# Kernel tuning notes

Hardware: AMD Instinct MI355X
Metric: run time of the kernel (lower is better)

## Reference

```python
import jax, jax.numpy as jnp
import numpy as np

N, C, H, E = 51200, 200, 128, 8
NE = N * 32
S_COEF, B_COEF = 0.01, 0.01
BN_EPS = 1e-5


def setup_inputs() -> dict:
    key = jax.random.key(0)
    ks = jax.random.split(key, 12)
    inp = {}
    inp["v"] = jax.random.normal(ks[0], (N, C), jnp.float32)
    inp["a_rows"] = jax.random.randint(ks[1], (NE,), 0, N, dtype=jnp.int32)
    inp["a_cols"] = jax.random.randint(ks[2], (NE,), 0, N, dtype=jnp.int32)
    inp["a_vals"] = jax.random.uniform(ks[3], (NE,), jnp.float32)
    inp["gate_W"] = jax.random.normal(ks[4], (C, E), jnp.float32) * 0.05
    inp["gate_b"] = jnp.zeros((E,), jnp.float32)
    inp["eps"] = jnp.zeros((E,), jnp.float32)  # GIN epsilon, init 0
    inp["W1"] = jax.random.normal(ks[5], (E, C, H), jnp.float32) / np.sqrt(C)
    inp["b1"] = jnp.zeros((E, H), jnp.float32)
    inp["g1"] = jnp.ones((E, H), jnp.float32)
    inp["beta1"] = jnp.zeros((E, H), jnp.float32)
    inp["W2"] = jax.random.normal(ks[6], (E, H, H), jnp.float32) / np.sqrt(H)
    inp["b2"] = jnp.zeros((E, H), jnp.float32)
    inp["g2"] = jnp.ones((E, H), jnp.float32)
    inp["beta2"] = jnp.zeros((E, H), jnp.float32)
    inp["b"] = 4
    inp["t"] = 64
    inp["n"] = 200
    return inp


def _bn_relu(h, g, beta):
    # h: [E, N, H]; batch-norm over node axis per expert (training-mode batch stats)
    mu = jnp.mean(h, axis=1, keepdims=True)
    var = jnp.var(h, axis=1, keepdims=True)
    hn = (h - mu) * jax.lax.rsqrt(var + BN_EPS)
    return jax.nn.relu(hn * g[:, None, :] + beta[:, None, :])


def reference(v, a_rows, a_cols, a_vals, gate_W, gate_b, eps,
              W1, b1, g1, beta1, W2, b2, g2, beta2, b, t, n):
    num_nodes, c = v.shape
    e = gate_W.shape[1]
    # ---- gating on x = rearrange(v, '(b t n) c -> b t n c') ----
    x = v.reshape(b, t, n, c)
    logits = jnp.einsum('btnc,ce->btne', x, gate_W) + gate_b
    probs = jax.nn.softmax(logits, axis=-1)                 # [b,t,n,E]
    top_val = jnp.max(probs, axis=-1, keepdims=True)
    top_idx = jnp.argmax(probs, axis=-1)
    gates = jax.nn.one_hot(top_idx, e, dtype=probs.dtype) * top_val  # top-1 sparse gates
    # ---- aux losses (switch-style balance; sparsity = mean top prob) ----
    probs_flat = probs.reshape(-1, e)
    gates_flat = gates.reshape(-1, e)
    importance = jnp.mean(probs_flat, axis=0)
    load = jnp.mean(jax.nn.one_hot(top_idx.reshape(-1), e, dtype=probs.dtype), axis=0)
    bal_loss = B_COEF * e * jnp.sum(importance * load)
    spa_loss = -S_COEF * jnp.mean(top_val)
    # ---- all-expert GIN compute (dense over experts, as in the torch loop) ----
    # shared sparse aggregation: agg[i] = sum_j a[i,j] * v[j]
    agg = jax.ops.segment_sum(a_vals[:, None] * v[a_cols], a_rows, num_segments=num_nodes)
    xin = agg[None] + (1.0 + eps)[:, None, None] * v[None]  # [E,N,C]
    h = jnp.einsum('enc,ech->enh', xin, W1) + b1[:, None, :]
    h = _bn_relu(h, g1, beta1)
    h = jnp.einsum('enk,ekh->enh', h, W2) + b2[:, None, :]
    h = _bn_relu(h, g2, beta2)                               # [E,N,H]
    # ---- gate-masked combine ----
    out = jnp.einsum('enh,ne->nh', h, gates_flat)            # [N,H]
    return out, (bal_loss, spa_loss)
```

## Files before the change

kernel.cpp:

```cpp
#include <hip/hip_runtime.h>


#define NNODES 51200
#define CDIM   200
#define CPAD   208
#define HDIM   128
#define NEXP   8
#define BNEPS  1e-5f
#define KC1    26
#define KS2    8
#define NB     400
#define CAP    6144
#define EPB    8192

typedef __attribute__((ext_vector_type(8)))  short short8;
typedef __attribute__((ext_vector_type(16))) float floatx16;
typedef unsigned short ushort_t;

__device__ __forceinline__ ushort_t f2bf(float x) {
  unsigned int u = __float_as_uint(x);
  u += 0x7fffu + ((u >> 16) & 1u);
  return (ushort_t)(u >> 16);
}
__device__ __forceinline__ float bf2f(ushort_t h) {
  return __uint_as_float(((unsigned int)h) << 16);
}

__global__ __launch_bounds__(256) void gating_kernel(
    const float* __restrict__ v, const float* __restrict__ gW,
    const float* __restrict__ gb, int* __restrict__ top_idx,
    float* __restrict__ top_val, ushort_t* __restrict__ v_bf,
    float* __restrict__ imp_acc, float* __restrict__ cnt_acc,
    float* __restrict__ tv_acc)
{
  __shared__ float s_imp[NEXP], s_cnt[NEXP], s_tv;
  const int tid = threadIdx.x, lane = tid & 63, wave = tid >> 6;
  if (tid < NEXP) { s_imp[tid] = 0.f; s_cnt[tid] = 0.f; }
  if (tid == 0) s_tv = 0.f;
  __syncthreads();
  const int c0 = lane * 4;
  const bool act = lane < 50;
  float gwr[4][NEXP];
#pragma unroll
  for (int r = 0; r < 4; ++r)
#pragma unroll
    for (int e = 0; e < NEXP; ++e)
      gwr[r][e] = act ? gW[(c0 + r) * NEXP + e] : 0.f;
  for (int i = 0; i < 16; ++i) {
    const int node = blockIdx.x * 64 + wave * 16 + i;
    float4 x = make_float4(0.f, 0.f, 0.f, 0.f);
    if (act) x = *(const float4*)(v + (size_t)node * CDIM + c0);
    float p[NEXP];
#pragma unroll
    for (int e = 0; e < NEXP; ++e)
      p[e] = fmaf(x.x, gwr[0][e],
             fmaf(x.y, gwr[1][e],
             fmaf(x.z, gwr[2][e], x.w * gwr[3][e])));
#pragma unroll
    for (int off = 32; off > 0; off >>= 1)
#pragma unroll
      for (int e = 0; e < NEXP; ++e) p[e] += __shfl_xor(p[e], off, 64);
#pragma unroll
    for (int e = 0; e < NEXP; ++e) p[e] += gb[e];
    if (lane < 52) {
      ushort4 o = {0, 0, 0, 0};
      if (act) { o.x = f2bf(x.x); o.y = f2bf(x.y); o.z = f2bf(x.z); o.w = f2bf(x.w); }
      *(ushort4*)(v_bf + (size_t)node * CPAD + c0) = o;
    }
    float mx = p[0]; int ai = 0;
#pragma unroll
    for (int e = 1; e < NEXP; ++e) if (p[e] > mx) { mx = p[e]; ai = e; }
    float se = 0.f, pe[NEXP];
#pragma unroll
    for (int e = 0; e < NEXP; ++e) { pe[e] = __expf(p[e] - mx); se += pe[e]; }
    const float inv = 1.f / se;
    if (lane == 0) {
      top_idx[node] = ai;
      top_val[node] = inv;
#pragma unroll
      for (int e = 0; e < NEXP; ++e) atomicAdd(&s_imp[e], pe[e] * inv);
      atomicAdd(&s_cnt[ai], 1.f);
      atomicAdd(&s_tv, inv);
    }
  }
  __syncthreads();
  if (tid < NEXP) { atomicAdd(&imp_acc[tid], s_imp[tid]); atomicAdd(&cnt_acc[tid], s_cnt[tid]); }
  if (tid == 0) atomicAdd(tv_acc, s_tv);
}

__global__ __launch_bounds__(256) void bucketA_kernel(
    const int* __restrict__ rows, const int* __restrict__ cols,
    const float* __restrict__ vals, int* __restrict__ bcnt,
    int2* __restrict__ tmp, int ne)
{
  __shared__ int cnt[NB];
  __shared__ int gbase[NB];
  const int tid = threadIdx.x;
  const int base = blockIdx.x * EPB;
  for (int b = tid; b < NB; b += 256) cnt[b] = 0;
  __syncthreads();
#pragma unroll 4
  for (int j = 0; j < EPB / 256; ++j) {
    const int i = base + j * 256 + tid;
    if (i < ne) atomicAdd(&cnt[rows[i] >> 7], 1);
  }
  __syncthreads();
  for (int b = tid; b < NB; b += 256) {
    const int c = cnt[b];
    gbase[b] = c ? (b * CAP + atomicAdd(&bcnt[b], c)) : 0;
    cnt[b] = 0;
  }
  __syncthreads();
#pragma unroll 4
  for (int j = 0; j < EPB / 256; ++j) {
    const int i = base + j * 256 + tid;
    if (i < ne) {
      const int r = rows[i];
      const int b = r >> 7;
      const int pos = gbase[b] + atomicAdd(&cnt[b], 1);
      tmp[pos] = make_int2((r << 16) | cols[i], __float_as_int(vals[i]));
    }
  }
}

__global__ __launch_bounds__(256) void bucketB_kernel(
    const int2* __restrict__ tmp, const int* __restrict__ bcnt,
    int2* __restrict__ cv, int* __restrict__ row_start, int* __restrict__ counts)
{
  __shared__ int lhist[128];
  __shared__ int lcur[128];
  const int tid = threadIdx.x;
  const int b = blockIdx.x;
  const int n = bcnt[b];
  const int base = b * CAP;
  int2 ed[CAP / 256];
#pragma unroll
  for (int j = 0; j < CAP / 256; ++j) {
    const int i = j * 256 + tid;
    if (i < n) ed[j] = tmp[base + i];
  }
  if (tid < 128) lhist[tid] = 0;
  __syncthreads();
#pragma unroll
  for (int j = 0; j < CAP / 256; ++j)
    if (j * 256 + tid < n)
      atomicAdd(&lhist[(((unsigned)ed[j].x) >> 16) & 127], 1);
  __syncthreads();
  if (tid == 0) {
    int acc = base;
    for (int r = 0; r < 128; ++r) { lcur[r] = acc; acc += lhist[r]; }
  }
  __syncthreads();
  if (tid < 128) {
    row_start[(b << 7) + tid] = lcur[tid];
    counts[(b << 7) + tid] = lhist[tid];
  }
  __syncthreads();
#pragma unroll
  for (int j = 0; j < CAP / 256; ++j)
    if (j * 256 + tid < n) {
      const int r = (((unsigned)ed[j].x) >> 16) & 127;
      const int pos = atomicAdd(&lcur[r], 1);
      cv[pos] = make_int2(ed[j].x & 0xffff, ed[j].y);
    }
}

__global__ __launch_bounds__(256) void aggregate_kernel(
    const ushort_t* __restrict__ v_bf, const int2* __restrict__ cv,
    const int* __restrict__ row_start, const int* __restrict__ counts,
    ushort_t* __restrict__ agg_bf)
{
  const int node = (blockIdx.x * 256 + threadIdx.x) >> 6;
  const int lane = threadIdx.x & 63;
  const int start = row_start[node];
  const int cnt   = counts[node];
  const bool act  = lane < 52;
  float4 a = make_float4(0.f, 0.f, 0.f, 0.f);
  int k = 0;
  for (; k + 8 <= cnt; k += 8) {
    int2 ee[8];
#pragma unroll
    for (int u = 0; u < 8; ++u) ee[u] = cv[start + k + u];
    ushort4 xx[8];
#pragma unroll
    for (int u = 0; u < 8; ++u) {
      ushort4 t = {0, 0, 0, 0};
      if (act) t = *(const ushort4*)(v_bf + (size_t)ee[u].x * CPAD + lane * 4);
      xx[u] = t;
    }
#pragma unroll
    for (int u = 0; u < 8; ++u) {
      const float vv = __int_as_float(ee[u].y);
      a.x = fmaf(vv, bf2f(xx[u].x), a.x);
      a.y = fmaf(vv, bf2f(xx[u].y), a.y);
      a.z = fmaf(vv, bf2f(xx[u].z), a.z);
      a.w = fmaf(vv, bf2f(xx[u].w), a.w);
    }
  }
  for (; k < cnt; ++k) {
    const int2 e0 = cv[start + k];
    ushort4 x0 = {0, 0, 0, 0};
    if (act) x0 = *(const ushort4*)(v_bf + (size_t)e0.x * CPAD + lane * 4);
    const float v0 = __int_as_float(e0.y);
    a.x = fmaf(v0, bf2f(x0.x), a.x); a.y = fmaf(v0, bf2f(x0.y), a.y);
    a.z = fmaf(v0, bf2f(x0.z), a.z); a.w = fmaf(v0, bf2f(x0.w), a.w);
  }
  if (act) {
    ushort4 o; o.x = f2bf(a.x); o.y = f2bf(a.y); o.z = f2bf(a.z); o.w = f2bf(a.w);
    *(ushort4*)(agg_bf + (size_t)node * CPAD + lane * 4) = o;
  }
}

__global__ __launch_bounds__(256) void btconv_all(
    const float* __restrict__ W1, const float* __restrict__ W2,
    const float* __restrict__ eps, ushort_t* __restrict__ Bt1,
    ushort_t* __restrict__ Bt2)
{
  const int e = blockIdx.y, j = blockIdx.x;
  __shared__ float tile[16][128];
  const int tid = threadIdx.x;
  const int kr = tid >> 5, n4 = (tid & 31) * 4;
  const float* W; int K, jj; float sc; ushort_t* dst;
  if (j < KC1) {
    sc = (j >= 13) ? (1.f + eps[e]) : 1.f;
    jj = (j >= 13) ? (j - 13) : j;
    W = W1; K = CDIM;
    dst = Bt1 + (((size_t)e * KC1 + j) * 256) * 8;
  } else {
    sc = 1.f; jj = j - KC1; W = W2; K = HDIM;
    dst = Bt2 + (((size_t)e * KS2 + jj) * 256) * 8;
  }
#pragma unroll
  for (int h = 0; h < 2; ++h) {
    const int k = jj * 16 + kr + h * 8;
    float4 val = make_float4(0.f, 0.f, 0.f, 0.f);
    if (k < K) val = *(const float4*)(W + ((size_t)e * K + k) * HDIM + n4);
    *(float4*)&tile[kr + h * 8][n4] = val;
  }
  __syncthreads();
  const int kh = tid >> 7, n = tid & 127;
  short8 pk;
#pragma unroll
  for (int q = 0; q < 8; ++q) pk[q] = (short)f2bf(sc * tile[kh * 8 + q][n]);
  *(short8*)(dst + (size_t)tid * 8) = pk;
}

__global__ __launch_bounds__(256, 2) void gemm1_mfma(
    const ushort_t* __restrict__ agg_bf, const ushort_t* __restrict__ v_bf,
    const ushort_t* __restrict__ Bt1x, ushort_t* __restrict__ h1,
    float* __restrict__ sum1, float* __restrict__ sq1)
{
  const int m0 = blockIdx.x * 64;
  __shared__ ushort_t sA[52 * 64 * 8];
  const int tid = threadIdx.x;
  const int lane = tid & 63, wid = tid >> 6;
  const int l31 = lane & 31, half = lane >> 5;

#pragma unroll
  for (int it = 0; it < 13; ++it) {
    const int l = it * 256 + tid;
    const int g = l >> 6, m = l & 63;
    const ushort_t* src = (g < 26)
        ? agg_bf + (size_t)(m0 + m) * CPAD + g * 8
        : v_bf  + (size_t)(m0 + m) * CPAD + (g - 26) * 8;
    *(short8*)(sA + (size_t)l * 8) = *(const short8*)src;
  }
  __syncthreads();

#pragma unroll
  for (int ei = 0; ei < 2; ++ei) {
    const int e = wid + ei * 4;
    floatx16 acc[2][4];
#pragma unroll
    for (int ms = 0; ms < 2; ++ms)
#pragma unroll
      for (int ns = 0; ns < 4; ++ns)
#pragma unroll
        for (int r = 0; r < 16; ++r) acc[ms][ns][r] = 0.f;

    const ushort_t* bte = Bt1x + ((size_t)e * KC1 * 256 + half * 128 + l31) * 8;
    short8 nb[4];
#pragma unroll
    for (int ns = 0; ns < 4; ++ns)
      nb[ns] = *(const short8*)(bte + (size_t)(ns * 32) * 8);
#pragma unroll
    for (int j = 0; j < KC1; ++j) {
      short8 b[4];
#pragma unroll
      for (int ns = 0; ns < 4; ++ns) b[ns] = nb[ns];
      if (j < KC1 - 1) {
#pragma unroll
        for (int ns = 0; ns < 4; ++ns)
          nb[ns] = *(const short8*)(bte + (size_t)((j + 1) * 256 + ns * 32) * 8);
      }
      short8 a[2];
#pragma unroll
      for (int ms = 0; ms < 2; ++ms)
        a[ms] = *(const short8*)(sA + (size_t)((2 * j + half) * 64 + ms * 32 + l31) * 8);
#pragma unroll
      for (int ms = 0; ms < 2; ++ms)
#pragma unroll
        for (int ns = 0; ns < 4; ++ns)
          acc[ms][ns] = __builtin_amdgcn_mfma_f32_32x32x16_bf16(
              a[ms], b[ns], acc[ms][ns], 0, 0, 0);
    }

    ushort_t* h1e = h1 + ((size_t)e * NNODES + m0) * HDIM;
#pragma unroll
    for (int ns = 0; ns < 4; ++ns) {
      const int col = ns * 32 + l31;
      float s = 0.f, q = 0.f;
#pragma unroll
      for (int ms = 0; ms < 2; ++ms) {
#pragma unroll
        for (int r = 0; r < 16; ++r) {
          const int row = ms * 32 + (r & 3) + 8 * (r >> 2) + 4 * half;
          const float x = acc[ms][ns][r];
          h1e[(size_t)row * HDIM + col] = f2bf(x);
          s += x; q = fmaf(x, x, q);
        }
      }
      s += __shfl_xor(s, 32, 64);
      q += __shfl_xor(q, 32, 64);
      if (half == 0) {
        atomicAdd(&sum1[e * HDIM + col], s);
        atomicAdd(&sq1[e * HDIM + col], q);
      }
    }
  }
}

__global__ __launch_bounds__(256, 4) void gemm2_mfma(
    const ushort_t* __restrict__ h1, const ushort_t* __restrict__ Bt2,
    const float* __restrict__ sum1, const float* __restrict__ sq1,
    const float* __restrict__ g1, const float* __restrict__ beta1,
    const int* __restrict__ top_idx, float* __restrict__ h2_sel,
    float* __restrict__ sum2, float* __restrict__ sq2)
{
  const int e = blockIdx.y;
  const int m0 = blockIdx.x * 128;
  __shared__ ushort_t sA[16 * 129 * 8];
  __shared__ float ssum[HDIM], ssq[HDIM];
  __shared__ float sSc[HDIM], sSh[HDIM];
  __shared__ int sTop[128];
  const int tid = threadIdx.x;
  const int lane = tid & 63, wid = tid >> 6;
  const int wm = wid >> 1, wn = wid & 1;
  const int l31 = lane & 31, half = lane >> 5;
  if (tid < HDIM) {
    ssum[tid] = 0.f; ssq[tid] = 0.f;
    sTop[tid] = top_idx[m0 + tid];
    const int i = e * HDIM + tid;
    const float invN = 1.f / (float)NNODES;
    const float mean = sum1[i] * invN;
    const float var  = sq1[i] * invN - mean * mean;
    const float sc = rsqrtf(var + BNEPS) * g1[i];
    sSc[tid] = sc;
    sSh[tid] = fmaf(-mean, sc, beta1[i]);
  }
  __syncthreads();
  {
    const int g = tid & 15, r0 = tid >> 4;
    const float4 sc0 = *(const float4*)&sSc[g * 8];
    const float4 sc1 = *(const float4*)&sSc[g * 8 + 4];
    const float4 sh0 = *(const float4*)&sSh[g * 8];
    const float4 sh1 = *(const float4*)&sSh[g * 8 + 4];
#pragma unroll
    for (int c = 0; c < 8; ++c) {
      const int m = c * 16 + r0;
      const short8 hq = *(const short8*)(
          h1 + ((size_t)e * NNODES + m0 + m) * HDIM + g * 8);
      short8 pk;
      pk[0] = (short)f2bf(fmaxf(0.f, fmaf(bf2f((ushort_t)hq[0]), sc0.x, sh0.x)));
      pk[1] = (short)f2bf(fmaxf(0.f, fmaf(bf2f((ushort_t)hq[1]), sc0.y, sh0.y)));
      pk[2] = (short)f2bf(fmaxf(0.f, fmaf(bf2f((ushort_t)hq[2]), sc0.z, sh0.z)));
      pk[3] = (short)f2bf(fmaxf(0.f, fmaf(bf2f((ushort_t)hq[3]), sc0.w, sh0.w)));
      pk[4] = (short)f2bf(fmaxf(0.f, fmaf(bf2f((ushort_t)hq[4]), sc1.x, sh1.x)));
      pk[5] = (short)f2bf(fmaxf(0.f, fmaf(bf2f((ushort_t)hq[5]), sc1.y, sh1.y)));
      pk[6] = (short)f2bf(fmaxf(0.f, fmaf(bf2f((ushort_t)hq[6]), sc1.z, sh1.z)));
      pk[7] = (short)f2bf(fmaxf(0.f, fmaf(bf2f((ushort_t)hq[7]), sc1.w, sh1.w)));
      *(short8*)(sA + (size_t)(g * 129 + m) * 8) = pk;
    }
  }
  __syncthreads();

  floatx16 acc[2][2];
#pragma unroll
  for (int i = 0; i < 2; ++i)
#pragma unroll
    for (int j = 0; j < 2; ++j)
#pragma unroll
      for (int r = 0; r < 16; ++r) acc[i][j][r] = 0.f;

  const ushort_t* bte = Bt2 + ((size_t)e * KS2 * 256 + half * 128 + wn * 64 + l31) * 8;
  short8 nb0 = *(const short8*)(bte);
  short8 nb1 = *(const short8*)(bte + 32 * 8);
#pragma unroll
  for (int ks = 0; ks < KS2; ++ks) {
    const short8 b0 = nb0, b1 = nb1;
    if (ks < KS2 - 1) {
      nb0 = *(const short8*)(bte + (size_t)((ks + 1) * 256) * 8);
      nb1 = *(const short8*)(bte + (size_t)((ks + 1) * 256 + 32) * 8);
    }
    const short8 a0 = *(const short8*)(sA + (size_t)((2 * ks + half) * 129 + wm * 64 + l31) * 8);
    const short8 a1 = *(const short8*)(sA + (size_t)((2 * ks + half) * 129 + wm * 64 + 32 + l31) * 8);
    acc[0][0] = __builtin_amdgcn_mfma_f32_32x32x16_bf16(a0, b0, acc[0][0], 0, 0, 0);
    acc[0][1] = __builtin_amdgcn_mfma_f32_32x32x16_bf16(a0, b1, acc[0][1], 0, 0, 0);
    acc[1][0] = __builtin_amdgcn_mfma_f32_32x32x16_bf16(a1, b0, acc[1][0], 0, 0, 0);
    acc[1][1] = __builtin_amdgcn_mfma_f32_32x32x16_bf16(a1, b1, acc[1][1], 0, 0, 0);
  }

#pragma unroll
  for (int ms = 0; ms < 2; ++ms)
#pragma unroll
    for (int ns = 0; ns < 2; ++ns) {
      const int col = wn * 64 + ns * 32 + l31;
      float s = 0.f, q = 0.f;
#pragma unroll
      for (int r = 0; r < 16; ++r) {
        const int row = wm * 64 + ms * 32 + (r & 3) + 8 * (r >> 2) + 4 * half;
        const float x = acc[ms][ns][r];
        if (sTop[row] == e) h2_sel[(size_t)(m0 + row) * HDIM + col] = x;
        s += x; q = fmaf(x, x, q);
      }
      atomicAdd(&ssum[col], s);
      atomicAdd(&ssq[col], q);
    }
  __syncthreads();
  if (tid < HDIM) atomicAdd(&sum2[e * HDIM + tid], ssum[tid]);
  else            atomicAdd(&sq2[e * HDIM + tid - HDIM], ssq[tid - HDIM]);
}

__global__ __launch_bounds__(256) void combine_kernel(
    const float* __restrict__ h2_sel, const int* __restrict__ top_idx,
    const float* __restrict__ top_val, const float* __restrict__ sum2,
    const float* __restrict__ sq2, const float* __restrict__ g2,
    const float* __restrict__ beta2, const float* __restrict__ imp,
    const float* __restrict__ cntv, const float* __restrict__ tv,
    float* __restrict__ out)
{
  __shared__ float s2[NEXP * HDIM], b2s[NEXP * HDIM];
  const int tid = threadIdx.x;
  const float invN = 1.f / (float)NNODES;
  for (int t = tid; t < NEXP * HDIM; t += 256) {
    const float mean = sum2[t] * invN;
    const float var  = sq2[t] * invN - mean * mean;
    const float sc = rsqrtf(var + BNEPS) * g2[t];
    s2[t] = sc;
    b2s[t] = fmaf(-mean, sc, beta2[t]);
  }
  __syncthreads();
  const int i4 = (blockIdx.x * 256 + tid) * 4;
  const int n = i4 >> 7, h = i4 & 127;
  const int e = top_idx[n];
  const float tvv = top_val[n];
  const float4 x = *(const float4*)(h2_sel + i4);
  const float* sc = s2 + e * HDIM + h;
  const float* sh = b2s + e * HDIM + h;
  float4 o;
  o.x = tvv * fmaxf(0.f, fmaf(x.x, sc[0], sh[0]));
  o.y = tvv * fmaxf(0.f, fmaf(x.y, sc[1], sh[1]));
  o.z = tvv * fmaxf(0.f, fmaf(x.z, sc[2], sh[2]));
  o.w = tvv * fmaxf(0.f, fmaf(x.w, sc[3], sh[3]));
  *(float4*)(out + i4) = o;
  if (blockIdx.x == 0 && tid == 0) {
    float bal = 0.f;
#pragma unroll
    for (int q = 0; q < NEXP; ++q) bal += (imp[q] * invN) * (cntv[q] * invN);
    out[(size_t)NNODES * HDIM]     = 0.01f * (float)NEXP * bal;
    out[(size_t)NNODES * HDIM + 1] = -0.01f * tv[0] * invN;
  }
}

struct WS {
  ushort_t *v_bf, *agg_bf, *h1, *Bt1x, *Bt2;
  float *h2_sel;
  int2 *cv, *tmp;
  int *row_start, *counts, *top_idx;
  float *top_val;
  char *zero_base; size_t zero_bytes;
  int *bcnt;
  float *sum1, *sq1, *sum2, *sq2, *imp, *cnt, *tv;
  size_t total;
};

static WS carve_ws(char* base)
{
  WS w; size_t off = 0;
  auto take = [&](size_t b) -> char* {
    char* r = base + off; off += (b + 255) & ~(size_t)255; return r;
  };
  w.v_bf   = (ushort_t*)take((size_t)NNODES * CPAD * 2);
  w.agg_bf = (ushort_t*)take((size_t)NNODES * CPAD * 2);
  w.h2_sel = (float*)w.v_bf;
  w.h1     = (ushort_t*)take((size_t)NEXP * NNODES * HDIM * 2);
  w.cv     = (int2*)take((size_t)NB * CAP * 8);
  w.tmp    = (int2*)take((size_t)NB * CAP * 8);
  w.Bt1x   = (ushort_t*)take((size_t)NEXP * KC1 * 2048 * 2);
  w.Bt2    = (ushort_t*)take((size_t)NEXP * KS2 * 2048 * 2);
  w.row_start = (int*)take(NNODES * 4);
  w.counts    = (int*)take(NNODES * 4);
  w.top_idx   = (int*)take(NNODES * 4);
  w.top_val   = (float*)take(NNODES * 4);
  w.zero_base = base + off;
  w.bcnt = (int*)take(NB * 4);
  w.sum1 = (float*)take(NEXP * HDIM * 4);
  w.sq1  = (float*)take(NEXP * HDIM * 4);
  w.sum2 = (float*)take(NEXP * HDIM * 4);
  w.sq2  = (float*)take(NEXP * HDIM * 4);
  w.imp  = (float*)take(NEXP * 4);
  w.cnt  = (float*)take(NEXP * 4);
  w.tv   = (float*)take(4);
  w.zero_bytes = (size_t)((base + off) - w.zero_base);
  w.total = off;
  return w;
}

extern "C" void kernel_launch(void* const* d_in, const int* in_sizes, int n_in,
                              void* d_out, int out_size, void* d_ws, size_t ws_size,
                              hipStream_t stream)
{
  const float* v      = (const float*)d_in[0];
  const int*   a_rows = (const int*)d_in[1];
  const int*   a_cols = (const int*)d_in[2];
  const float* a_vals = (const float*)d_in[3];
  const float* gate_W = (const float*)d_in[4];
  const float* gate_b = (const float*)d_in[5];
  const float* eps    = (const float*)d_in[6];
  const float* W1     = (const float*)d_in[7];
  const float* g1     = (const float*)d_in[9];
  const float* beta1  = (const float*)d_in[10];
  const float* W2     = (const float*)d_in[11];
  const float* g2     = (const float*)d_in[13];
  const float* beta2  = (const float*)d_in[14];
  const int NE = in_sizes[1];
  float* out = (float*)d_out;
  (void)n_in; (void)out_size; (void)ws_size;

  WS w = carve_ws((char*)d_ws);

  hipMemsetAsync(w.zero_base, 0, w.zero_bytes, stream);

  gating_kernel<<<NNODES / 64, 256, 0, stream>>>(
      v, gate_W, gate_b, w.top_idx, w.top_val, w.v_bf, w.imp, w.cnt, w.tv);
  btconv_all<<<dim3(KC1 + KS2, NEXP), 256, 0, stream>>>(
      W1, W2, eps, w.Bt1x, w.Bt2);
  bucketA_kernel<<<(NE + EPB - 1) / EPB, 256, 0, stream>>>(
      a_rows, a_cols, a_vals, w.bcnt, w.tmp, NE);
  bucketB_kernel<<<NB, 256, 0, stream>>>(
      w.tmp, w.bcnt, w.cv, w.row_start, w.counts);
  aggregate_kernel<<<NNODES / 4, 256, 0, stream>>>(
      w.v_bf, w.cv, w.row_start, w.counts, w.agg_bf);

  gemm1_mfma<<<NNODES / 64, 256, 0, stream>>>(
      w.agg_bf, w.v_bf, w.Bt1x, w.h1, w.sum1, w.sq1);
  gemm2_mfma<<<dim3(NNODES / 128, NEXP), 256, 0, stream>>>(
      w.h1, w.Bt2, w.sum1, w.sq1, g1, beta1, w.top_idx,
      w.h2_sel, w.sum2, w.sq2);
  combine_kernel<<<(NNODES * HDIM) / 1024, 256, 0, stream>>>(
      w.h2_sel, w.top_idx, w.top_val, w.sum2, w.sq2, g2, beta2,
      w.imp, w.cnt, w.tv, out);
}
```

Measured before the change: 543.7 us.

## Fuse sparse neighbor aggregation into gemm1 shared-memory prologue

Removes the standalone aggregate kernel and computes each node's sparse neighbor sum directly into gemm1's shared-memory A tile, alongside the node's own features, using a row-major padded layout. This avoids writing and re-reading the bf16 aggregate buffer in global memory and one kernel launch. In exchange, the latency-bound gathers now run inside the GEMM blocks with fewer waves in flight and a smaller unroll, which may hurt latency hiding. h2_sel gets its own buffer instead of aliasing v_bf.

```diff
diff --git a/kernel.cpp b/kernel.cpp
--- a/kernel.cpp
+++ b/kernel.cpp
@@ -12,6 +12,7 @@
 #define NB     400
 #define CAP    6144
 #define EPB    8192
+#define ASTR   428
 
 typedef __attribute__((ext_vector_type(8)))  short short8;
 typedef __attribute__((ext_vector_type(16))) float floatx16;
@@ -163,52 +164,6 @@
       const int pos = atomicAdd(&lcur[r], 1);
       cv[pos] = make_int2(ed[j].x & 0xffff, ed[j].y);
     }
-}
-
-__global__ __launch_bounds__(256) void aggregate_kernel(
-    const ushort_t* __restrict__ v_bf, const int2* __restrict__ cv,
-    const int* __restrict__ row_start, const int* __restrict__ counts,
-    ushort_t* __restrict__ agg_bf)
-{
-  const int node = (blockIdx.x * 256 + threadIdx.x) >> 6;
-  const int lane = threadIdx.x & 63;
-  const int start = row_start[node];
-  const int cnt   = counts[node];
-  const bool act  = lane < 52;
-  float4 a = make_float4(0.f, 0.f, 0.f, 0.f);
-  int k = 0;
-  for (; k + 8 <= cnt; k += 8) {
-    int2 ee[8];
-#pragma unroll
-    for (int u = 0; u < 8; ++u) ee[u] = cv[start + k + u];
-    ushort4 xx[8];
-#pragma unroll
-    for (int u = 0; u < 8; ++u) {
-      ushort4 t = {0, 0, 0, 0};
-      if (act) t = *(const ushort4*)(v_bf + (size_t)ee[u].x * CPAD + lane * 4);
-      xx[u] = t;
-    }
-#pragma unroll
-    for (int u = 0; u < 8; ++u) {
-      const float vv = __int_as_float(ee[u].y);
-      a.x = fmaf(vv, bf2f(xx[u].x), a.x);
-      a.y = fmaf(vv, bf2f(xx[u].y), a.y);
-      a.z = fmaf(vv, bf2f(xx[u].z), a.z);
-      a.w = fmaf(vv, bf2f(xx[u].w), a.w);
-    }
-  }
-  for (; k < cnt; ++k) {
-    const int2 e0 = cv[start + k];
-    ushort4 x0 = {0, 0, 0, 0};
-    if (act) x0 = *(const ushort4*)(v_bf + (size_t)e0.x * CPAD + lane * 4);
-    const float v0 = __int_as_float(e0.y);
-    a.x = fmaf(v0, bf2f(x0.x), a.x); a.y = fmaf(v0, bf2f(x0.y), a.y);
-    a.z = fmaf(v0, bf2f(x0.z), a.z); a.w = fmaf(v0, bf2f(x0.w), a.w);
-  }
-  if (act) {
-    ushort4 o; o.x = f2bf(a.x); o.y = f2bf(a.y); o.z = f2bf(a.z); o.w = f2bf(a.w);
-    *(ushort4*)(agg_bf + (size_t)node * CPAD + lane * 4) = o;
-  }
 }
 
 __global__ __launch_bounds__(256) void btconv_all(
@@ -246,24 +201,63 @@
 }
 
 __global__ __launch_bounds__(256, 2) void gemm1_mfma(
-    const ushort_t* __restrict__ agg_bf, const ushort_t* __restrict__ v_bf,
+    const ushort_t* __restrict__ v_bf, const int2* __restrict__ cv,
+    const int* __restrict__ row_start, const int* __restrict__ counts,
     const ushort_t* __restrict__ Bt1x, ushort_t* __restrict__ h1,
     float* __restrict__ sum1, float* __restrict__ sq1)
 {
   const int m0 = blockIdx.x * 64;
-  __shared__ ushort_t sA[52 * 64 * 8];
+  __shared__ ushort_t sA[64 * ASTR];
   const int tid = threadIdx.x;
   const int lane = tid & 63, wid = tid >> 6;
   const int l31 = lane & 31, half = lane >> 5;
-
-#pragma unroll
-  for (int it = 0; it < 13; ++it) {
-    const int l = it * 256 + tid;
-    const int g = l >> 6, m = l & 63;
-    const ushort_t* src = (g < 26)
-        ? agg_bf + (size_t)(m0 + m) * CPAD + g * 8
-        : v_bf  + (size_t)(m0 + m) * CPAD + (g - 26) * 8;
-    *(short8*)(sA + (size_t)l * 8) = *(const short8*)src;
+  const bool act = lane < 52;
+
+  for (int rr = 0; rr < 16; ++rr) {
+    const int m = wid * 16 + rr;
+    const int node = m0 + m;
+    if (act)
+      *(ushort4*)(sA + (size_t)m * ASTR + 208 + lane * 4) =
+          *(const ushort4*)(v_bf + (size_t)node * CPAD + lane * 4);
+    const int start = row_start[node];
+    const int cnt   = counts[node];
+    float4 a = make_float4(0.f, 0.f, 0.f, 0.f);
+    int k = 0;
+    for (; k + 4 <= cnt; k += 4) {
+      const int2 e0 = cv[start + k];
+      const int2 e1 = cv[start + k + 1];
+      const int2 e2 = cv[start + k + 2];
+      const int2 e3 = cv[start + k + 3];
+      ushort4 x0 = {0,0,0,0}, x1 = {0,0,0,0}, x2 = {0,0,0,0}, x3 = {0,0,0,0};
+      if (act) {
+        x0 = *(const ushort4*)(v_bf + (size_t)e0.x * CPAD + lane * 4);
+        x1 = *(const ushort4*)(v_bf + (size_t)e1.x * CPAD + lane * 4);
+        x2 = *(const ushort4*)(v_bf + (size_t)e2.x * CPAD + lane * 4);
+        x3 = *(const ushort4*)(v_bf + (size_t)e3.x * CPAD + lane * 4);
+      }
+      const float v0 = __int_as_float(e0.y), v1 = __int_as_float(e1.y);
+      const float v2 = __int_as_float(e2.y), v3 = __int_as_float(e3.y);
+      a.x = fmaf(v0, bf2f(x0.x), a.x); a.y = fmaf(v0, bf2f(x0.y), a.y);
+      a.z = fmaf(v0, bf2f(x0.z), a.z); a.w = fmaf(v0, bf2f(x0.w), a.w);
+      a.x = fmaf(v1, bf2f(x1.x), a.x); a.y = fmaf(v1, bf2f(x1.y), a.y);
+      a.z = fmaf(v1, bf2f(x1.z), a.z); a.w = fmaf(v1, bf2f(x1.w), a.w);
+      a.x = fmaf(v2, bf2f(x2.x), a.x); a.y = fmaf(v2, bf2f(x2.y), a.y);
+      a.z = fmaf(v2, bf2f(x2.z), a.z); a.w = fmaf(v2, bf2f(x2.w), a.w);
+      a.x = fmaf(v3, bf2f(x3.x), a.x); a.y = fmaf(v3, bf2f(x3.y), a.y);
+      a.z = fmaf(v3, bf2f(x3.z), a.z); a.w = fmaf(v3, bf2f(x3.w), a.w);
+    }
+    for (; k < cnt; ++k) {
+      const int2 e0 = cv[start + k];
+      ushort4 x0 = {0, 0, 0, 0};
+      if (act) x0 = *(const ushort4*)(v_bf + (size_t)e0.x * CPAD + lane * 4);
+      const float v0 = __int_as_float(e0.y);
+      a.x = fmaf(v0, bf2f(x0.x), a.x); a.y = fmaf(v0, bf2f(x0.y), a.y);
+      a.z = fmaf(v0, bf2f(x0.z), a.z); a.w = fmaf(v0, bf2f(x0.w), a.w);
+    }
+    if (act) {
+      ushort4 o; o.x = f2bf(a.x); o.y = f2bf(a.y); o.z = f2bf(a.z); o.w = f2bf(a.w);
+      *(ushort4*)(sA + (size_t)m * ASTR + lane * 4) = o;
+    }
   }
   __syncthreads();
 
@@ -296,7 +290,7 @@
       short8 a[2];
 #pragma unroll
       for (int ms = 0; ms < 2; ++ms)
-        a[ms] = *(const short8*)(sA + (size_t)((2 * j + half) * 64 + ms * 32 + l31) * 8);
+        a[ms] = *(const short8*)(sA + (size_t)(ms * 32 + l31) * ASTR + (2 * j + half) * 8);
 #pragma unroll
       for (int ms = 0; ms < 2; ++ms)
 #pragma unroll
@@ -473,7 +467,7 @@
 }
 
 struct WS {
-  ushort_t *v_bf, *agg_bf, *h1, *Bt1x, *Bt2;
+  ushort_t *v_bf, *h1, *Bt1x, *Bt2;
   float *h2_sel;
   int2 *cv, *tmp;
   int *row_start, *counts, *top_idx;
@@ -491,8 +485,7 @@
     char* r = base + off; off += (b + 255) & ~(size_t)255; return r;
   };
   w.v_bf   = (ushort_t*)take((size_t)NNODES * CPAD * 2);
-  w.agg_bf = (ushort_t*)take((size_t)NNODES * CPAD * 2);
-  w.h2_sel = (float*)w.v_bf;
+  w.h2_sel = (float*)take((size_t)NNODES * HDIM * 4);
   w.h1     = (ushort_t*)take((size_t)NEXP * NNODES * HDIM * 2);
   w.cv     = (int2*)take((size_t)NB * CAP * 8);
   w.tmp    = (int2*)take((size_t)NB * CAP * 8);
@@ -549,11 +542,9 @@
       a_rows, a_cols, a_vals, w.bcnt, w.tmp, NE);
   bucketB_kernel<<<NB, 256, 0, stream>>>(
       w.tmp, w.bcnt, w.cv, w.row_start, w.counts);
-  aggregate_kernel<<<NNODES / 4, 256, 0, stream>>>(
-      w.v_bf, w.cv, w.row_start, w.counts, w.agg_bf);
 
   gemm1_mfma<<<NNODES / 64, 256, 0, stream>>>(
-      w.agg_bf, w.v_bf, w.Bt1x, w.h1, w.sum1, w.sq1);
+      w.v_bf, w.cv, w.row_start, w.counts, w.Bt1x, w.h1, w.sum1, w.sq1);
   gemm2_mfma<<<dim3(NNODES / 128, NEXP), 256, 0, stream>>>(
       w.h1, w.Bt2, w.sum1, w.sq1, g1, beta1, w.top_idx,
       w.h2_sel, w.sum2, w.sq2);
```

Result: slower. 644.4 us (+18.5%).
